# Optimization experiments

Hardware: AMD Instinct MI355X
Metric: run time of the kernel (lower is better)

Reference implementation:

```python
import jax, jax.numpy as jnp
import numpy as np

B, L = 1, 384
D_EDGE, D_BIAS, N_HEAD, D_HEAD = 128, 64, 4, 48
INF = 1000000.0
SCALE = 1.0 / np.sqrt(D_HEAD)
EPS = 1e-5


def _layernorm(x, g, b):
    mu = jnp.mean(x, axis=-1, keepdims=True)
    var = jnp.mean(jnp.square(x - mu), axis=-1, keepdims=True)
    return (x - mu) * jax.lax.rsqrt(var + EPS) * g + b


def _rope(x, pos):
    # x: [B, n, L, h, d], pos: [B, L] integer positions along the attended (i/j) axis
    half = x.shape[-1] // 2
    inv_freq = 1.0 / (10000.0 ** (jnp.arange(half, dtype=jnp.float32) / half))
    ang = pos.astype(jnp.float32)[..., None] * inv_freq          # [B, L, half]
    cos = jnp.cos(ang)[:, None, :, None, :]                       # [B,1,L,1,half]
    sin = jnp.sin(ang)[:, None, :, None, :]
    x1, x2 = jnp.split(x, 2, axis=-1)
    return jnp.concatenate([x1 * cos - x2 * sin, x1 * sin + x2 * cos], axis=-1)


def setup_inputs() -> dict:
    key = jax.random.key(0)
    ks = jax.random.split(key, 10)
    s = 0.02
    return {
        "edge": jax.random.normal(ks[0], (B, L, L, D_EDGE), jnp.float32),
        "bias": jax.random.normal(ks[1], (B, L, L, D_BIAS), jnp.float32),
        "edge_pos": jnp.arange(B * L, dtype=jnp.int32).reshape(B, L),
        "edge_mask": jnp.ones((B, L, L), jnp.float32),
        "ln_e_g": jnp.ones((D_EDGE,), jnp.float32),
        "ln_e_b": jnp.zeros((D_EDGE,), jnp.float32),
        "ln_b_g": jnp.ones((D_BIAS,), jnp.float32),
        "ln_b_b": jnp.zeros((D_BIAS,), jnp.float32),
        "Wq": jax.random.normal(ks[2], (D_EDGE, N_HEAD * D_HEAD), jnp.float32) * s,
        "Wk": jax.random.normal(ks[3], (D_EDGE, N_HEAD * D_HEAD), jnp.float32) * s,
        "Wv": jax.random.normal(ks[4], (D_EDGE, N_HEAD * D_HEAD), jnp.float32) * s,
        "Wb": jax.random.normal(ks[5], (D_BIAS, N_HEAD), jnp.float32) * s,
        "Wg": jax.random.normal(ks[6], (D_EDGE, N_HEAD * D_HEAD), jnp.float32) * s,
        "bg": jnp.zeros((N_HEAD * D_HEAD,), jnp.float32),
        "Wo": jax.random.normal(ks[7], (N_HEAD * D_HEAD, D_EDGE), jnp.float32) * s,
    }


def reference(edge, bias, edge_pos, edge_mask, ln_e_g, ln_e_b, ln_b_g, ln_b_b,
              Wq, Wk, Wv, Wb, Wg, bg, Wo):
    # is_row=True: swap the two residue axes of the pair representation
    e = jnp.transpose(edge, (0, 2, 1, 3))
    bi = jnp.transpose(bias, (0, 2, 1, 3))
    e = _layernorm(e, ln_e_g, ln_e_b)
    bi = _layernorm(bi, ln_b_g, ln_b_b)

    def proj(x, W):
        return (x @ W).reshape(B, L, L, N_HEAD, D_HEAD)

    q = proj(e, Wq)                      # [B, n, i, h, d]
    k = proj(e, Wk)
    v = proj(e, Wv)
    q = _rope(q, edge_pos)
    k = _rope(k, edge_pos)
    b_h = bi @ Wb                        # [B, i, j, h]
    gate = jax.nn.sigmoid(proj(e, Wg) + bg.reshape(1, 1, 1, N_HEAD, D_HEAD))

    q = q * SCALE
    k = k / L
    attn = jnp.einsum('bnihk,bnjhk->bijh', q, k) + b_h
    attn = jax.nn.softmax(attn, axis=-2)                 # softmax over j (dim -2)
    attn = attn + (INF * (edge_mask - 1.0))[..., None]    # post-softmax additive mask

    out = jnp.einsum('bijh,bnjhd->bnihd', attn, v)        # [B, n, i, h, d]
    out = gate * out
    out = out.reshape(B, L, L, N_HEAD * D_HEAD) @ Wo      # [B, n, i, d_edge]
    return jnp.transpose(out, (0, 2, 1, 3))               # undo row permute
```

## Files before the change

### kernel.cpp

```cpp
#include <hip/hip_runtime.h>
#include <hip/hip_bf16.h>


#define LQ 384
#define DE 128
#define DBI 64
#define DH 48
#define NPOS (LQ*LQ)
#define KQK (LQ*DH)

typedef __attribute__((ext_vector_type(8))) short short8;
typedef __attribute__((ext_vector_type(4))) float f32x4;
typedef unsigned short u16;
typedef unsigned int u32;

__device__ __forceinline__ float b2f(u16 u) {
  union { u32 i; float f; } v; v.i = ((u32)u) << 16; return v.f;
}
__device__ __forceinline__ u16 f2b(float f) {
  __hip_bfloat16 h = __float2bfloat16(f);
  return __builtin_bit_cast(unsigned short, h);
}
__device__ __forceinline__ float wred_sum(float v) {
  #pragma unroll
  for (int o = 32; o; o >>= 1) v += __shfl_down(v, o);
  return __shfl(v, 0);
}

__device__ __forceinline__ void gemm_128x192(
    const u16* __restrict__ A, long lda, const u16* __restrict__ B, long ldb,
    int kTiles, u16* sA, u16* sB, f32x4 (&acc)[4][6])
{
  const int t = threadIdx.x;
  const int w = t >> 6, lane = t & 63, quad = lane >> 4, l16 = lane & 15;
  const int wr = w >> 1, wc = w & 1;
  for (int kt = 0; kt < kTiles; ++kt) {
    #pragma unroll
    for (int r = 0; r < 4; ++r) {
      int id = t + r * 256, row = id >> 3, c8 = (id & 7) * 8;
      *(uint4*)(sA + row * 72 + c8) = *(const uint4*)(A + (long)row * lda + kt * 64 + c8);
    }
    #pragma unroll
    for (int r = 0; r < 6; ++r) {
      int id = t + r * 256, row = id >> 3, c8 = (id & 7) * 8;
      *(uint4*)(sB + row * 72 + c8) = *(const uint4*)(B + (long)row * ldb + kt * 64 + c8);
    }
    __syncthreads();
    #pragma unroll
    for (int kk = 0; kk < 64; kk += 32) {
      short8 a[4], bf[6];
      #pragma unroll
      for (int rr = 0; rr < 4; ++rr)
        a[rr] = *(const short8*)(sA + (wr * 64 + rr * 16 + l16) * 72 + kk + quad * 8);
      #pragma unroll
      for (int f = 0; f < 6; ++f)
        bf[f] = *(const short8*)(sB + (wc * 96 + f * 16 + l16) * 72 + kk + quad * 8);
      #pragma unroll
      for (int rr = 0; rr < 4; ++rr)
        #pragma unroll
        for (int f = 0; f < 6; ++f)
          acc[rr][f] = __builtin_amdgcn_mfma_f32_16x16x32_bf16(a[rr], bf[f], acc[rr][f], 0, 0, 0);
    }
    __syncthreads();
  }
}

__global__ __launch_bounds__(256) void k_prep_w(
    const float* __restrict__ Wq, const float* __restrict__ Wk,
    const float* __restrict__ Wv, const float* __restrict__ Wg,
    const float* __restrict__ Wo, const int* __restrict__ epos,
    u16* __restrict__ WT, u16* __restrict__ WoT,
    float* __restrict__ cosT, float* __restrict__ sinT)
{
  int idx = blockIdx.x * 256 + threadIdx.x;
  if (idx < 768 * 128) {
    int col = idx >> 7, c = idx & 127;
    int which = col / 192, wi = col % 192;
    const float* W = (which == 0) ? Wq : (which == 1) ? Wk : (which == 2) ? Wv : Wg;
    WT[(long)col * 128 + c] = f2b(W[(long)c * 192 + wi]);
  }
  if (idx < 128 * 192) {
    int c = idx / 192, col = idx % 192;
    WoT[(long)c * 192 + col] = f2b(Wo[(long)col * 128 + c]);
  }
  if (idx < 384 * 24) {
    int i2 = idx / 24, dd = idx % 24;
    float ang = (float)epos[i2] * exp2f((float)dd * (-13.287712379549449f / 24.f));
    cosT[idx] = cosf(ang);
    sinT[idx] = sinf(ang);
  }
}

__global__ __launch_bounds__(256) void k_ln_e(
    const float* __restrict__ edge, const float* __restrict__ g,
    const float* __restrict__ b, u16* __restrict__ e_ln)
{
  int w = threadIdx.x >> 6, lane = threadIdx.x & 63;
  long p = (long)blockIdx.x * 4 + w;
  int n = (int)(p / LQ), i2 = (int)(p % LQ);
  const float* src = edge + ((long)i2 * LQ + n) * DE;
  float2 x = *(const float2*)(src + lane * 2);
  float mu = wred_sum(x.x + x.y) * (1.f / 128.f);
  float ms = wred_sum(x.x * x.x + x.y * x.y) * (1.f / 128.f);
  float r = rsqrtf(ms - mu * mu + 1e-5f);
  int c = lane * 2;
  u16 y0 = f2b((x.x - mu) * r * g[c] + b[c]);
  u16 y1 = f2b((x.y - mu) * r * g[c + 1] + b[c + 1]);
  *(u32*)(e_ln + p * DE + c) = (u32)y0 | ((u32)y1 << 16);
}

__global__ __launch_bounds__(256) void k_bias(
    const float* __restrict__ bias, const float* __restrict__ g,
    const float* __restrict__ b, const float* __restrict__ Wb,
    float* __restrict__ logits)
{
  int w = threadIdx.x >> 6, lane = threadIdx.x & 63;
  long q = (long)blockIdx.x * 4 + w;
  int i = (int)(q / LQ), j = (int)(q % LQ);
  float x = bias[((long)j * LQ + i) * DBI + lane];
  float mu = wred_sum(x) * (1.f / 64.f);
  float ms = wred_sum(x * x) * (1.f / 64.f);
  float r = rsqrtf(ms - mu * mu + 1e-5f);
  float y = (x - mu) * r * g[lane] + b[lane];
  #pragma unroll
  for (int h = 0; h < 4; ++h) {
    float v = y * Wb[lane * 4 + h];
    #pragma unroll
    for (int o = 32; o; o >>= 1) v += __shfl_down(v, o);
    if (lane == 0) logits[((long)h * LQ + i) * LQ + j] = v;
  }
}

__global__ __launch_bounds__(256) void k_proj(
    const u16* __restrict__ e_ln, const u16* __restrict__ WT,
    const float* __restrict__ cosT, const float* __restrict__ sinT,
    const float* __restrict__ bg,
    u16* __restrict__ q_buf, u16* __restrict__ k_buf,
    u16* __restrict__ vT, u16* __restrict__ gate)
{
  __shared__ __align__(16) u16 sA[128 * 136];
  __shared__ __align__(16) char sU[128 * 49 * 4];
  const int t = threadIdx.x;
  const int w = t >> 6, lane = t & 63, quad = lane >> 4, l16 = lane & 15;
  long mt = blockIdx.x;
  long pbase = mt * 128;
  int n = (int)(pbase / LQ), i2base = (int)(pbase % LQ);

  #pragma unroll
  for (int r = 0; r < 8; ++r) {
    int id = t + r * 256, row = id >> 4, c8 = (id & 15) * 8;
    *(uint4*)(sA + row * 136 + c8) = *(const uint4*)(e_ln + (pbase + row) * DE + c8);
  }
  __syncthreads();
  short8 a[2][4];
  #pragma unroll
  for (int rr = 0; rr < 2; ++rr)
    #pragma unroll
    for (int kki = 0; kki < 4; ++kki)
      a[rr][kki] = *(const short8*)(sA + (w * 32 + rr * 16 + l16) * 136 + kki * 32 + quad * 8);

  for (int cc = 0; cc < 16; ++cc) {
    int which = cc >> 2, h = cc & 3;
    u16* sB = (u16*)sU;
    #pragma unroll
    for (int r = 0; r < 3; ++r) {
      int id = t + r * 256, row = id >> 4, c8 = (id & 15) * 8;
      *(uint4*)(sB + row * 136 + c8) = *(const uint4*)(WT + ((long)cc * 48 + row) * DE + c8);
    }
    __syncthreads();
    f32x4 acc[2][3] = {};
    #pragma unroll
    for (int kki = 0; kki < 4; ++kki)
      #pragma unroll
      for (int f = 0; f < 3; ++f) {
        short8 bf = *(const short8*)(sB + (f * 16 + l16) * 136 + kki * 32 + quad * 8);
        acc[0][f] = __builtin_amdgcn_mfma_f32_16x16x32_bf16(a[0][kki], bf, acc[0][f], 0, 0, 0);
        acc[1][f] = __builtin_amdgcn_mfma_f32_16x16x32_bf16(a[1][kki], bf, acc[1][f], 0, 0, 0);
      }
    __syncthreads();
    float* sC = (float*)sU;
    #pragma unroll
    for (int rr = 0; rr < 2; ++rr)
      #pragma unroll
      for (int f = 0; f < 3; ++f)
        #pragma unroll
        for (int r = 0; r < 4; ++r)
          sC[(w * 32 + rr * 16 + quad * 4 + r) * 49 + f * 16 + l16] = acc[rr][f][r];
    __syncthreads();
    if (which < 2) {
      float scl = (which == 0) ? 0.14433756729740643f : (1.0f / 384.0f);
      u16* dst = (which == 0) ? q_buf : k_buf;
      int row = t >> 1, half = t & 1;
      int i2 = i2base + row;
      const float* ct = cosT + i2 * 24;
      const float* st = sinT + i2 * 24;
      long base = ((long)(h * LQ + i2) * LQ + n) * DH;
      #pragma unroll
      for (int kd = 0; kd < 24; kd += 2) {
        u16 y2[2];
        #pragma unroll
        for (int u = 0; u < 2; ++u) {
          int d = half * 24 + kd + u;
          int dd = (d < 24) ? d : d - 24;
          float cs = ct[dd], sn = st[dd];
          float x1 = sC[row * 49 + dd], x2 = sC[row * 49 + dd + 24];
          float y = (d < 24) ? (x1 * cs - x2 * sn) : (x1 * sn + x2 * cs);
          y2[u] = f2b(y * scl);
        }
        *(u32*)(dst + base + half * 24 + kd) = (u32)y2[0] | ((u32)y2[1] << 16);
      }
    } else if (which == 2) {
      for (int e = t; e < 6144; e += 256) {
        int d = e >> 7, row = e & 127;
        vT[((long)h * KQK + n * DH + d) * LQ + (i2base + row)] = f2b(sC[row * 49 + d]);
      }
    } else {
      for (int e = t; e < 6144; e += 256) {
        int row = e / 48, d = e - row * 48;
        float xx = sC[row * 49 + d] + bg[h * DH + d];
        gate[(pbase + row) * 192 + h * DH + d] = f2b(1.f / (1.f + expf(-xx)));
      }
    }
    __syncthreads();
  }
}

__global__ __launch_bounds__(256) void k_qk(
    const u16* __restrict__ q_buf, const u16* __restrict__ k_buf,
    float* __restrict__ logits)
{
  __shared__ __align__(16) u16 sA[128 * 72];
  __shared__ __align__(16) u16 sB[192 * 72];
  int nt = blockIdx.x & 1, s = blockIdx.x >> 1;
  int mt = blockIdx.y, h = blockIdx.z;
  f32x4 acc[4][6] = {};
  gemm_128x192(q_buf + ((long)h * LQ + mt * 128) * KQK + s * 576, KQK,
               k_buf + ((long)h * LQ + nt * 192) * KQK + s * 576, KQK,
               9, sA, sB, acc);
  const int t = threadIdx.x;
  const int w = t >> 6, lane = t & 63, quad = lane >> 4, l16 = lane & 15;
  const int wr = w >> 1, wc = w & 1;
  #pragma unroll
  for (int rr = 0; rr < 4; ++rr)
    #pragma unroll
    for (int f = 0; f < 6; ++f)
      #pragma unroll
      for (int r = 0; r < 4; ++r) {
        int row = mt * 128 + wr * 64 + rr * 16 + quad * 4 + r;
        int col = nt * 192 + wc * 96 + f * 16 + l16;
        atomicAdd(logits + ((long)h * LQ + row) * LQ + col, acc[rr][f][r]);
      }
}

__global__ __launch_bounds__(256) void k_softmax(
    const float* __restrict__ logits, const float* __restrict__ mask,
    u16* __restrict__ attn)
{
  int w = threadIdx.x >> 6, lane = threadIdx.x & 63;
  long row = (long)blockIdx.x * 4 + w;
  int i = (int)(row % LQ);
  const float* src = logits + row * LQ;
  float v[6];
  float mx = -1e30f;
  #pragma unroll
  for (int j0 = 0; j0 < 6; ++j0) { v[j0] = src[lane + j0 * 64]; mx = fmaxf(mx, v[j0]); }
  #pragma unroll
  for (int o = 32; o; o >>= 1) mx = fmaxf(mx, __shfl_down(mx, o));
  mx = __shfl(mx, 0);
  float s = 0.f;
  #pragma unroll
  for (int j0 = 0; j0 < 6; ++j0) { v[j0] = expf(v[j0] - mx); s += v[j0]; }
  s = wred_sum(s);
  float inv = 1.f / s;
  #pragma unroll
  for (int j0 = 0; j0 < 6; ++j0) {
    int j = lane + j0 * 64;
    float p = v[j0] * inv + 1.0e6f * (mask[(long)i * LQ + j] - 1.f);
    attn[row * LQ + j] = f2b(p);
  }
}

__global__ __launch_bounds__(256) void k_av(
    const u16* __restrict__ attn, const u16* __restrict__ vT,
    u16* __restrict__ out_buf)
{
  __shared__ __align__(16) u16 sA[128 * 72];
  __shared__ __align__(16) u16 sB[192 * 72];
  int nt = blockIdx.x, mt = blockIdx.y, h = blockIdx.z;
  f32x4 acc[4][6] = {};
  gemm_128x192(attn + ((long)h * LQ + mt * 128) * LQ, LQ,
               vT + ((long)h * KQK + nt * 192) * LQ, LQ,
               6, sA, sB, acc);
  const int t = threadIdx.x;
  const int w = t >> 6, lane = t & 63, quad = lane >> 4, l16 = lane & 15;
  const int wr = w >> 1, wc = w & 1;
  #pragma unroll
  for (int rr = 0; rr < 4; ++rr)
    #pragma unroll
    for (int f = 0; f < 6; ++f)
      #pragma unroll
      for (int r = 0; r < 4; ++r) {
        int i = mt * 128 + wr * 64 + rr * 16 + quad * 4 + r;
        int C = nt * 192 + wc * 96 + f * 16 + l16;
        int nn = C / 48, d = C - nn * 48;
        out_buf[((long)nn * LQ + i) * 192 + h * DH + d] = f2b(acc[rr][f][r]);
      }
}

__global__ __launch_bounds__(256) void k_out(
    const u16* __restrict__ out_buf, const u16* __restrict__ gate,
    const u16* __restrict__ WoT, float* __restrict__ outp)
{
  __shared__ __align__(16) u16 sA[128 * 72];
  __shared__ __align__(16) u16 sB[128 * 72];
  long mt = blockIdx.x;
  const int t = threadIdx.x;
  const int w = t >> 6, lane = t & 63, quad = lane >> 4, l16 = lane & 15;
  const int wr = w >> 1, wc = w & 1;
  f32x4 acc[4][4] = {};
  const u16* A1 = out_buf + mt * 128 * 192;
  const u16* A2 = gate + mt * 128 * 192;
  for (int kt = 0; kt < 3; ++kt) {
    #pragma unroll
    for (int r = 0; r < 4; ++r) {
      int id = t + r * 256, row = id >> 3, c8 = (id & 7) * 8;
      long off = (long)row * 192 + kt * 64 + c8;
      union { u16 s[8]; uint4 v; } ua, ub, ur;
      ua.v = *(const uint4*)(A1 + off);
      ub.v = *(const uint4*)(A2 + off);
      #pragma unroll
      for (int q2 = 0; q2 < 8; ++q2) ur.s[q2] = f2b(b2f(ua.s[q2]) * b2f(ub.s[q2]));
      *(uint4*)(sA + row * 72 + c8) = ur.v;
    }
    #pragma unroll
    for (int r = 0; r < 4; ++r) {
      int id = t + r * 256, row = id >> 3, c8 = (id & 7) * 8;
      *(uint4*)(sB + row * 72 + c8) = *(const uint4*)(WoT + (long)row * 192 + kt * 64 + c8);
    }
    __syncthreads();
    #pragma unroll
    for (int kk = 0; kk < 64; kk += 32) {
      short8 a[4], bf[4];
      #pragma unroll
      for (int rr = 0; rr < 4; ++rr)
        a[rr] = *(const short8*)(sA + (wr * 64 + rr * 16 + l16) * 72 + kk + quad * 8);
      #pragma unroll
      for (int f = 0; f < 4; ++f)
        bf[f] = *(const short8*)(sB + (wc * 64 + f * 16 + l16) * 72 + kk + quad * 8);
      #pragma unroll
      for (int rr = 0; rr < 4; ++rr)
        #pragma unroll
        for (int f = 0; f < 4; ++f)
          acc[rr][f] = __builtin_amdgcn_mfma_f32_16x16x32_bf16(a[rr], bf[f], acc[rr][f], 0, 0, 0);
    }
    __syncthreads();
  }
  long pbase = mt * 128;
  int n = (int)(pbase / LQ), ibase = (int)(pbase % LQ);
  #pragma unroll
  for (int rr = 0; rr < 4; ++rr)
    #pragma unroll
    for (int f = 0; f < 4; ++f)
      #pragma unroll
      for (int r = 0; r < 4; ++r) {
        int row = wr * 64 + rr * 16 + quad * 4 + r;
        int c = wc * 64 + f * 16 + l16;
        outp[((long)(ibase + row) * LQ + n) * DE + c] = acc[rr][f][r];
      }
}

extern "C" void kernel_launch(void* const* d_in, const int* in_sizes, int n_in,
                              void* d_out, int out_size, void* d_ws, size_t ws_size,
                              hipStream_t stream)
{
  const float* edge   = (const float*)d_in[0];
  const float* bias   = (const float*)d_in[1];
  const int*   epos   = (const int*)d_in[2];
  const float* mask   = (const float*)d_in[3];
  const float* ln_e_g = (const float*)d_in[4];
  const float* ln_e_b = (const float*)d_in[5];
  const float* ln_b_g = (const float*)d_in[6];
  const float* ln_b_b = (const float*)d_in[7];
  const float* Wq = (const float*)d_in[8];
  const float* Wk = (const float*)d_in[9];
  const float* Wv = (const float*)d_in[10];
  const float* Wb = (const float*)d_in[11];
  const float* Wg = (const float*)d_in[12];
  const float* bg = (const float*)d_in[13];
  const float* Wo = (const float*)d_in[14];
  float* outp = (float*)d_out;

  char* ws = (char*)d_ws;
  const size_t SZ = (size_t)NPOS * 192 * 2;
  u16* e_ln    = (u16*)ws;
  u16* out_buf = (u16*)ws;
  u16* q_buf   = (u16*)(ws + SZ);
  u16* k_buf   = (u16*)(ws + 2 * SZ);
  u16* vTb     = (u16*)(ws + 3 * SZ);
  u16* gateb   = (u16*)(ws + 4 * SZ);
  float* logits= (float*)(ws + 5 * SZ);
  u16* attn    = (u16*)(ws + 5 * SZ + 2359296);
  u16* WT      = (u16*)(ws + 5 * SZ + 2359296 + 1179648);
  u16* WoT     = (u16*)(ws + 5 * SZ + 2359296 + 1179648 + 196608);
  float* cosT  = (float*)(ws + 5 * SZ + 2359296 + 1179648 + 196608 + 49152);
  float* sinT  = cosT + 384 * 24;

  k_prep_w<<<dim3(384), dim3(256), 0, stream>>>(Wq, Wk, Wv, Wg, Wo, epos, WT, WoT, cosT, sinT);
  k_ln_e<<<dim3(36864), dim3(256), 0, stream>>>(edge, ln_e_g, ln_e_b, e_ln);
  k_bias<<<dim3(36864), dim3(256), 0, stream>>>(bias, ln_b_g, ln_b_b, Wb, logits);
  k_proj<<<dim3(1152), dim3(256), 0, stream>>>(e_ln, WT, cosT, sinT, bg, q_buf, k_buf, vTb, gateb);
  k_qk<<<dim3(64, 3, 4), dim3(256), 0, stream>>>(q_buf, k_buf, logits);
  k_softmax<<<dim3(384), dim3(256), 0, stream>>>(logits, mask, attn);
  k_av<<<dim3(96, 3, 4), dim3(256), 0, stream>>>(attn, vTb, out_buf);
  k_out<<<dim3(1152), dim3(256), 0, stream>>>(out_buf, gateb, WoT, outp);
}
```

Baseline: 579.1 us.

## Fuse edge layernorm into projection and replace atomic split-K with partial buffers

Removes the separate edge layernorm kernel by computing the layernorm inside the projection kernel straight into shared memory. This avoids writing and re-reading the bf16 normalized buffer. The QK split-K now uses 24 slices that write plain partial sums to a workspace instead of atomically adding into logits. Softmax then adds those partials to a separate bias buffer. Projection epilogues switch to 16-byte vectorized stores and fast exp. The cost is extra partial-buffer traffic (24 fp32 slices of logits) read back in softmax, and the projection loads are now strided fp32 rows.

```diff
diff --git a/kernel.cpp b/kernel.cpp
--- a/kernel.cpp
+++ b/kernel.cpp
@@ -5,6 +5,7 @@
 #define LQ 384
 #define DE 128
 #define DBI 64
+#define NH 4
 #define DH 48
 #define NPOS (LQ*LQ)
 #define KQK (LQ*DH)
@@ -91,28 +92,10 @@
   }
 }
 
-__global__ __launch_bounds__(256) void k_ln_e(
-    const float* __restrict__ edge, const float* __restrict__ g,
-    const float* __restrict__ b, u16* __restrict__ e_ln)
-{
-  int w = threadIdx.x >> 6, lane = threadIdx.x & 63;
-  long p = (long)blockIdx.x * 4 + w;
-  int n = (int)(p / LQ), i2 = (int)(p % LQ);
-  const float* src = edge + ((long)i2 * LQ + n) * DE;
-  float2 x = *(const float2*)(src + lane * 2);
-  float mu = wred_sum(x.x + x.y) * (1.f / 128.f);
-  float ms = wred_sum(x.x * x.x + x.y * x.y) * (1.f / 128.f);
-  float r = rsqrtf(ms - mu * mu + 1e-5f);
-  int c = lane * 2;
-  u16 y0 = f2b((x.x - mu) * r * g[c] + b[c]);
-  u16 y1 = f2b((x.y - mu) * r * g[c + 1] + b[c + 1]);
-  *(u32*)(e_ln + p * DE + c) = (u32)y0 | ((u32)y1 << 16);
-}
-
 __global__ __launch_bounds__(256) void k_bias(
     const float* __restrict__ bias, const float* __restrict__ g,
     const float* __restrict__ b, const float* __restrict__ Wb,
-    float* __restrict__ logits)
+    float* __restrict__ bh)
 {
   int w = threadIdx.x >> 6, lane = threadIdx.x & 63;
   long q = (long)blockIdx.x * 4 + w;
@@ -127,12 +110,14 @@
     float v = y * Wb[lane * 4 + h];
     #pragma unroll
     for (int o = 32; o; o >>= 1) v += __shfl_down(v, o);
-    if (lane == 0) logits[((long)h * LQ + i) * LQ + j] = v;
+    if (lane == 0) bh[((long)h * LQ + i) * LQ + j] = v;
   }
 }
 
 __global__ __launch_bounds__(256) void k_proj(
-    const u16* __restrict__ e_ln, const u16* __restrict__ WT,
+    const float* __restrict__ edge, const float* __restrict__ ln_g,
+    const float* __restrict__ ln_b,
+    const u16* __restrict__ WT,
     const float* __restrict__ cosT, const float* __restrict__ sinT,
     const float* __restrict__ bg,
     u16* __restrict__ q_buf, u16* __restrict__ k_buf,
@@ -146,12 +131,26 @@
   long pbase = mt * 128;
   int n = (int)(pbase / LQ), i2base = (int)(pbase % LQ);
 
-  #pragma unroll
-  for (int r = 0; r < 8; ++r) {
-    int id = t + r * 256, row = id >> 4, c8 = (id & 15) * 8;
-    *(uint4*)(sA + row * 136 + c8) = *(const uint4*)(e_ln + (pbase + row) * DE + c8);
+  {
+    int c = lane * 2;
+    float g0 = ln_g[c], g1 = ln_g[c + 1];
+    float b0 = ln_b[c], b1 = ln_b[c + 1];
+    #pragma unroll 2
+    for (int rr = 0; rr < 32; ++rr) {
+      int row = w * 32 + rr;
+      int i2 = i2base + row;
+      const float* src = edge + ((long)i2 * LQ + n) * DE;
+      float2 x = *(const float2*)(src + c);
+      float mu = wred_sum(x.x + x.y) * (1.f / 128.f);
+      float ms = wred_sum(x.x * x.x + x.y * x.y) * (1.f / 128.f);
+      float r = rsqrtf(ms - mu * mu + 1e-5f);
+      u16 y0 = f2b((x.x - mu) * r * g0 + b0);
+      u16 y1 = f2b((x.y - mu) * r * g1 + b1);
+      *(u32*)(sA + row * 136 + c) = (u32)y0 | ((u32)y1 << 16);
+    }
   }
   __syncthreads();
+
   short8 a[2][4];
   #pragma unroll
   for (int rr = 0; rr < 2; ++rr)
@@ -187,38 +186,51 @@
         for (int r = 0; r < 4; ++r)
           sC[(w * 32 + rr * 16 + quad * 4 + r) * 49 + f * 16 + l16] = acc[rr][f][r];
     __syncthreads();
+
     if (which < 2) {
       float scl = (which == 0) ? 0.14433756729740643f : (1.0f / 384.0f);
       u16* dst = (which == 0) ? q_buf : k_buf;
-      int row = t >> 1, half = t & 1;
-      int i2 = i2base + row;
-      const float* ct = cosT + i2 * 24;
-      const float* st = sinT + i2 * 24;
-      long base = ((long)(h * LQ + i2) * LQ + n) * DH;
-      #pragma unroll
-      for (int kd = 0; kd < 24; kd += 2) {
-        u16 y2[2];
-        #pragma unroll
-        for (int u = 0; u < 2; ++u) {
-          int d = half * 24 + kd + u;
+      #pragma unroll
+      for (int it = 0; it < 3; ++it) {
+        int id = t + it * 256;
+        int row = id / 6, c8 = (id % 6) * 8;
+        int i2 = i2base + row;
+        const float* ct = cosT + i2 * 24;
+        const float* st = sinT + i2 * 24;
+        union { u16 s[8]; uint4 v; } o;
+        #pragma unroll
+        for (int u = 0; u < 8; ++u) {
+          int d = c8 + u;
           int dd = (d < 24) ? d : d - 24;
-          float cs = ct[dd], sn = st[dd];
           float x1 = sC[row * 49 + dd], x2 = sC[row * 49 + dd + 24];
-          float y = (d < 24) ? (x1 * cs - x2 * sn) : (x1 * sn + x2 * cs);
-          y2[u] = f2b(y * scl);
+          float y = (d < 24) ? (x1 * ct[dd] - x2 * st[dd]) : (x1 * st[dd] + x2 * ct[dd]);
+          o.s[u] = f2b(y * scl);
         }
-        *(u32*)(dst + base + half * 24 + kd) = (u32)y2[0] | ((u32)y2[1] << 16);
+        *(uint4*)(dst + ((long)(h * LQ + i2) * LQ + n) * DH + c8) = o.v;
       }
     } else if (which == 2) {
-      for (int e = t; e < 6144; e += 256) {
-        int d = e >> 7, row = e & 127;
-        vT[((long)h * KQK + n * DH + d) * LQ + (i2base + row)] = f2b(sC[row * 49 + d]);
+      #pragma unroll
+      for (int it = 0; it < 3; ++it) {
+        int id = t + it * 256;
+        int d = id >> 4, j8 = (id & 15) * 8;
+        union { u16 s[8]; uint4 v; } o;
+        #pragma unroll
+        for (int u = 0; u < 8; ++u) o.s[u] = f2b(sC[(j8 + u) * 49 + d]);
+        *(uint4*)(vT + ((long)h * KQK + n * DH + d) * LQ + i2base + j8) = o.v;
       }
     } else {
-      for (int e = t; e < 6144; e += 256) {
-        int row = e / 48, d = e - row * 48;
-        float xx = sC[row * 49 + d] + bg[h * DH + d];
-        gate[(pbase + row) * 192 + h * DH + d] = f2b(1.f / (1.f + expf(-xx)));
+      #pragma unroll
+      for (int it = 0; it < 3; ++it) {
+        int id = t + it * 256;
+        int row = id / 6, c8 = (id % 6) * 8;
+        union { u16 s[8]; uint4 v; } o;
+        #pragma unroll
+        for (int u = 0; u < 8; ++u) {
+          int d = c8 + u;
+          float xx = sC[row * 49 + d] + bg[h * DH + d];
+          o.s[u] = f2b(1.f / (1.f + __expf(-xx)));
+        }
+        *(uint4*)(gate + (pbase + row) * 192 + h * DH + c8) = o.v;
       }
     }
     __syncthreads();
@@ -227,19 +239,20 @@
 
 __global__ __launch_bounds__(256) void k_qk(
     const u16* __restrict__ q_buf, const u16* __restrict__ k_buf,
-    float* __restrict__ logits)
+    float* __restrict__ partial)
 {
   __shared__ __align__(16) u16 sA[128 * 72];
   __shared__ __align__(16) u16 sB[192 * 72];
   int nt = blockIdx.x & 1, s = blockIdx.x >> 1;
   int mt = blockIdx.y, h = blockIdx.z;
   f32x4 acc[4][6] = {};
-  gemm_128x192(q_buf + ((long)h * LQ + mt * 128) * KQK + s * 576, KQK,
-               k_buf + ((long)h * LQ + nt * 192) * KQK + s * 576, KQK,
-               9, sA, sB, acc);
+  gemm_128x192(q_buf + ((long)h * LQ + mt * 128) * KQK + s * 768, KQK,
+               k_buf + ((long)h * LQ + nt * 192) * KQK + s * 768, KQK,
+               12, sA, sB, acc);
   const int t = threadIdx.x;
   const int w = t >> 6, lane = t & 63, quad = lane >> 4, l16 = lane & 15;
   const int wr = w >> 1, wc = w & 1;
+  float* dst = partial + ((long)s * NH + h) * NPOS;
   #pragma unroll
   for (int rr = 0; rr < 4; ++rr)
     #pragma unroll
@@ -248,30 +261,36 @@
       for (int r = 0; r < 4; ++r) {
         int row = mt * 128 + wr * 64 + rr * 16 + quad * 4 + r;
         int col = nt * 192 + wc * 96 + f * 16 + l16;
-        atomicAdd(logits + ((long)h * LQ + row) * LQ + col, acc[rr][f][r]);
+        dst[(long)row * LQ + col] = acc[rr][f][r];
       }
 }
 
 __global__ __launch_bounds__(256) void k_softmax(
-    const float* __restrict__ logits, const float* __restrict__ mask,
-    u16* __restrict__ attn)
+    const float* __restrict__ partial, const float* __restrict__ bh,
+    const float* __restrict__ mask, u16* __restrict__ attn)
 {
   int w = threadIdx.x >> 6, lane = threadIdx.x & 63;
   long row = (long)blockIdx.x * 4 + w;
   int i = (int)(row % LQ);
-  const float* src = logits + row * LQ;
   float v[6];
+  #pragma unroll
+  for (int j0 = 0; j0 < 6; ++j0) v[j0] = bh[row * LQ + lane + j0 * 64];
+  for (int s = 0; s < 24; ++s) {
+    const float* p = partial + (long)s * NH * NPOS + row * LQ;
+    #pragma unroll
+    for (int j0 = 0; j0 < 6; ++j0) v[j0] += p[lane + j0 * 64];
+  }
   float mx = -1e30f;
   #pragma unroll
-  for (int j0 = 0; j0 < 6; ++j0) { v[j0] = src[lane + j0 * 64]; mx = fmaxf(mx, v[j0]); }
+  for (int j0 = 0; j0 < 6; ++j0) mx = fmaxf(mx, v[j0]);
   #pragma unroll
   for (int o = 32; o; o >>= 1) mx = fmaxf(mx, __shfl_down(mx, o));
   mx = __shfl(mx, 0);
-  float s = 0.f;
-  #pragma unroll
-  for (int j0 = 0; j0 < 6; ++j0) { v[j0] = expf(v[j0] - mx); s += v[j0]; }
-  s = wred_sum(s);
-  float inv = 1.f / s;
+  float sum = 0.f;
+  #pragma unroll
+  for (int j0 = 0; j0 < 6; ++j0) { v[j0] = __expf(v[j0] - mx); sum += v[j0]; }
+  sum = wred_sum(sum);
+  float inv = 1.f / sum;
   #pragma unroll
   for (int j0 = 0; j0 < 6; ++j0) {
     int j = lane + j0 * 64;
@@ -392,13 +411,13 @@
 
   char* ws = (char*)d_ws;
   const size_t SZ = (size_t)NPOS * 192 * 2;
-  u16* e_ln    = (u16*)ws;
+  float* partial = (float*)ws;
   u16* out_buf = (u16*)ws;
   u16* q_buf   = (u16*)(ws + SZ);
   u16* k_buf   = (u16*)(ws + 2 * SZ);
   u16* vTb     = (u16*)(ws + 3 * SZ);
   u16* gateb   = (u16*)(ws + 4 * SZ);
-  float* logits= (float*)(ws + 5 * SZ);
+  float* bh    = (float*)(ws + 5 * SZ);
   u16* attn    = (u16*)(ws + 5 * SZ + 2359296);
   u16* WT      = (u16*)(ws + 5 * SZ + 2359296 + 1179648);
   u16* WoT     = (u16*)(ws + 5 * SZ + 2359296 + 1179648 + 196608);
@@ -406,11 +425,11 @@
   float* sinT  = cosT + 384 * 24;
 
   k_prep_w<<<dim3(384), dim3(256), 0, stream>>>(Wq, Wk, Wv, Wg, Wo, epos, WT, WoT, cosT, sinT);
-  k_ln_e<<<dim3(36864), dim3(256), 0, stream>>>(edge, ln_e_g, ln_e_b, e_ln);
-  k_bias<<<dim3(36864), dim3(256), 0, stream>>>(bias, ln_b_g, ln_b_b, Wb, logits);
-  k_proj<<<dim3(1152), dim3(256), 0, stream>>>(e_ln, WT, cosT, sinT, bg, q_buf, k_buf, vTb, gateb);
-  k_qk<<<dim3(64, 3, 4), dim3(256), 0, stream>>>(q_buf, k_buf, logits);
-  k_softmax<<<dim3(384), dim3(256), 0, stream>>>(logits, mask, attn);
+  k_bias<<<dim3(36864), dim3(256), 0, stream>>>(bias, ln_b_g, ln_b_b, Wb, bh);
+  k_proj<<<dim3(1152), dim3(256), 0, stream>>>(edge, ln_e_g, ln_e_b, WT, cosT, sinT, bg,
+                                               q_buf, k_buf, vTb, gateb);
+  k_qk<<<dim3(48, 3, 4), dim3(256), 0, stream>>>(q_buf, k_buf, partial);
+  k_softmax<<<dim3(384), dim3(256), 0, stream>>>(partial, bh, mask, attn);
   k_av<<<dim3(96, 3, 4), dim3(256), 0, stream>>>(attn, vTb, out_buf);
   k_out<<<dim3(1152), dim3(256), 0, stream>>>(out_buf, gateb, WoT, outp);
 }
```

Measured after the change: 652.0 us. 12.6% more time.
